# Kernel optimization log

Measured on AMD Instinct MI355X. Metric: run time of the kernel, lower is better.

## Reference

```python
import jax, jax.numpy as jnp
import numpy as np
from jax import lax


def _dense_image_warp(img, flow):
    # TFA semantics: out[b,i,j] = bilinear_sample(img[b], (i - flow[b,i,j,0], j - flow[b,i,j,1]))
    # floors clamped to [0, size-2]; alphas clamped to [0, 1].
    B, H, W, C = img.shape
    gy = jnp.arange(H, dtype=flow.dtype)[None, :, None]
    gx = jnp.arange(W, dtype=flow.dtype)[None, None, :]
    qy = gy - flow[..., 0]
    qx = gx - flow[..., 1]
    fy = jnp.clip(jnp.floor(qy), 0.0, H - 2)
    fx = jnp.clip(jnp.floor(qx), 0.0, W - 2)
    ay = jnp.clip(qy - fy, 0.0, 1.0)[..., None]
    ax = jnp.clip(qx - fx, 0.0, 1.0)[..., None]
    fy = fy.astype(jnp.int32)
    fx = fx.astype(jnp.int32)
    b = jnp.arange(B)[:, None, None]
    tl = img[b, fy, fx]
    tr = img[b, fy, fx + 1]
    bl = img[b, fy + 1, fx]
    br = img[b, fy + 1, fx + 1]
    top = tl + ax * (tr - tl)
    bot = bl + ax * (br - bl)
    return top + ay * (bot - top)


def _conv(x, w, b, act):
    y = lax.conv_general_dilated(x, w, (1, 1), 'SAME',
                                 dimension_numbers=('NHWC', 'HWIO', 'NHWC')) + b
    return jax.nn.relu(y) if act else y


def _predict(x, ws, bs):
    for i in range(4):
        x = _conv(x, ws[i], bs[i], True)
    return _conv(x, ws[4], bs[4], False)  # final 1x1 -> 2 channels, linear


def _upsample2x(x):
    B, H, W, C = x.shape
    return jax.image.resize(x, (B, 2 * H, 2 * W, C), method='bilinear')


# Conv stack dims: in=64 (concat of two 32-ch maps)
_KSHAPES = [(3, 3, 64, 32), (3, 3, 32, 64), (1, 1, 64, 64), (1, 1, 64, 16), (1, 1, 16, 2)]


def setup_inputs() -> dict:
    key = jax.random.key(0)
    ks = jax.random.split(key, 4 + 2 * len(_KSHAPES))
    B, H, W, C = 8, 256, 256, 32
    inp = {
        'input_1': jax.random.normal(ks[0], (B, H, W, C), jnp.float32),
        'input_2': jax.random.normal(ks[1], (B, H, W, C), jnp.float32),
        'flow_1_2': jax.random.normal(ks[2], (B, H, W, 2), jnp.float32) * 3.0,
        'flow_2_1': jax.random.normal(ks[3], (B, H, W, 2), jnp.float32) * 3.0,
    }
    for i, sh in enumerate(_KSHAPES):
        inp[f'w12_{i}'] = jax.random.normal(ks[4 + i], sh, jnp.float32) * 0.05
        inp[f'b12_{i}'] = jnp.zeros((sh[-1],), jnp.float32)
        inp[f'w21_{i}'] = jax.random.normal(ks[4 + len(_KSHAPES) + i], sh, jnp.float32) * 0.05
        inp[f'b21_{i}'] = jnp.zeros((sh[-1],), jnp.float32)
    return inp


def reference(input_1, input_2, flow_1_2, flow_2_1,
              w12_0, b12_0, w12_1, b12_1, w12_2, b12_2, w12_3, b12_3, w12_4, b12_4,
              w21_0, b21_0, w21_1, b21_1, w21_2, b21_2, w21_3, b21_3, w21_4, b21_4):
    ws12 = [w12_0, w12_1, w12_2, w12_3, w12_4]
    bs12 = [b12_0, b12_1, b12_2, b12_3, b12_4]
    ws21 = [w21_0, w21_1, w21_2, w21_3, w21_4]
    bs21 = [b21_0, b21_1, b21_2, b21_3, b21_4]

    # 1 -> 2 direction
    input_1_warped_1 = _dense_image_warp(input_1, flow_1_2)
    flow_change_1_2 = _predict(jnp.concatenate([input_2, input_1_warped_1], axis=3), ws12, bs12)
    flow_1_2_changed = flow_1_2 + flow_change_1_2
    input_1_warped_2 = _dense_image_warp(input_1, flow_1_2_changed)
    flow_1_2_up = _upsample2x(flow_1_2_changed)

    # 2 -> 1 direction
    input_2_warped_1 = _dense_image_warp(input_2, flow_2_1)
    flow_change_2_1 = _predict(jnp.concatenate([input_1, input_2_warped_1], axis=3), ws21, bs21)
    flow_2_1_changed = flow_2_1 + flow_change_2_1
    input_2_warped_2 = _dense_image_warp(input_2, flow_2_1_changed)
    flow_2_1_up = _upsample2x(flow_2_1_changed)

    return (input_1_warped_2, input_2_warped_2, flow_1_2_up, flow_2_1_up)
```

## Files before the change

kernel.cpp:

```cpp
#include <hip/hip_runtime.h>
#include <hip/hip_bf16.h>
#include <cstddef>

#define B_ 8
#define H_ 256
#define W_ 256

static constexpr int NPIX = B_ * H_ * W_;

typedef __attribute__((ext_vector_type(8))) short bf16x8;
typedef __attribute__((ext_vector_type(4))) float f32x4;

__device__ __forceinline__ float4 ld4(const float* p) { return *(const float4*)p; }

__device__ __forceinline__ short f2bf(float x) {
    unsigned u = __float_as_uint(x);
    unsigned r = (u + 0x7fffu + ((u >> 16) & 1u)) >> 16;
    return (short)r;
}

__global__ __launch_bounds__(256) void cvt_inputs_kernel(
    const float* __restrict__ in1, const float* __restrict__ in2,
    short* __restrict__ xb1, short* __restrict__ xb2)
{
    int t = blockIdx.x * 256 + threadIdx.x;
    const int N8 = NPIX * 32 / 8;
    const float* src = (t < N8) ? in1 : in2;
    short* dst = (t < N8) ? xb1 : xb2;
    int i = (t < N8) ? t : t - N8;
    float4 a = ld4(src + (size_t)i * 8);
    float4 b = ld4(src + (size_t)i * 8 + 4);
    bf16x8 r;
    r[0] = f2bf(a.x); r[1] = f2bf(a.y); r[2] = f2bf(a.z); r[3] = f2bf(a.w);
    r[4] = f2bf(b.x); r[5] = f2bf(b.y); r[6] = f2bf(b.z); r[7] = f2bf(b.w);
    *(bf16x8*)(dst + (size_t)i * 8) = r;
}

__global__ __launch_bounds__(256) void prep_weights_kernel(
    const float* __restrict__ w0a, const float* __restrict__ w1a,
    const float* __restrict__ w2a, const float* __restrict__ w3a,
    const float* __restrict__ w0b, const float* __restrict__ w1b,
    const float* __restrict__ w2b, const float* __restrict__ w3b,
    short* __restrict__ wt0, short* __restrict__ wt1)
{
    int t = blockIdx.x * 256 + threadIdx.x;
    if (t >= 2 * 5248) return;
    int dir = t / 5248;
    int r = t % 5248;
    const float* w0 = dir ? w0b : w0a;
    const float* w1 = dir ? w1b : w1a;
    const float* w2 = dir ? w2b : w2a;
    const float* w3 = dir ? w3b : w3a;
    short* wt = dir ? wt1 : wt0;
    bf16x8 v;
    if (r < 2304) {
        int l = r & 63, n = (r >> 6) & 1, c = (r >> 7) & 1, tp = r >> 8;
#pragma unroll
        for (int j = 0; j < 8; ++j) {
            int ci = c * 32 + 8 * (l >> 4) + j;
            int co = n * 16 + (l & 15);
            v[j] = f2bf(w0[(size_t)(tp * 64 + ci) * 32 + co]);
        }
    } else if (r < 4608) {
        int q = r - 2304;
        int l = q & 63, n = (q >> 6) & 3, tp = q >> 8;
#pragma unroll
        for (int j = 0; j < 8; ++j) {
            int ci = 8 * (l >> 4) + j;
            int co = n * 16 + (l & 15);
            v[j] = f2bf(w1[(size_t)(tp * 32 + ci) * 64 + co]);
        }
    } else if (r < 5120) {
        int q = r - 4608;
        int l = q & 63, n = (q >> 6) & 3, c = q >> 8;
#pragma unroll
        for (int j = 0; j < 8; ++j) {
            int k = 32 * c + 8 * (l >> 4) + j;
            int co = n * 16 + (l & 15);
            v[j] = f2bf(w2[(size_t)k * 64 + co]);
        }
    } else {
        int q = r - 5120;
        int l = q & 63, c = q >> 6;
#pragma unroll
        for (int j = 0; j < 8; ++j) {
            int k = 32 * c + 8 * (l >> 4) + j;
            v[j] = f2bf(w3[(size_t)k * 16 + (l & 15)]);
        }
    }
    *(bf16x8*)(wt + (size_t)r * 8) = v;
}

__global__ __launch_bounds__(256) void warp_bf16_kernel(
    const float* __restrict__ in1, const float* __restrict__ in2,
    const float* __restrict__ fl12, const float* __restrict__ fl21,
    short* __restrict__ wbf)
{
    int gid = blockIdx.x * 256 + threadIdx.x;
    int d   = (gid >= NPIX * 8);
    int g2  = gid - (d ? NPIX * 8 : 0);
    const float* img  = d ? in2 : in1;
    const float* flow = d ? fl21 : fl12;
    short* out = wbf + (size_t)d * NPIX * 32;

    int p   = g2 >> 3;
    int c4  = (g2 & 7) << 2;
    int b   = p >> 16;
    int i   = (p >> 8) & 255;
    int j   = p & 255;
    float2 f = *(const float2*)(flow + (size_t)p * 2);
    float qy = (float)i - f.x;
    float qx = (float)j - f.y;
    float fyf = fminf(fmaxf(floorf(qy), 0.0f), (float)(H_ - 2));
    float fxf = fminf(fmaxf(floorf(qx), 0.0f), (float)(W_ - 2));
    float ay = fminf(fmaxf(qy - fyf, 0.0f), 1.0f);
    float ax = fminf(fmaxf(qx - fxf, 0.0f), 1.0f);
    int fy = (int)fyf, fx = (int)fxf;
    const float* base = img + ((((size_t)b * H_ + fy) * W_ + fx) << 5) + c4;
    float4 tl = ld4(base);
    float4 tr = ld4(base + 32);
    float4 bl = ld4(base + W_ * 32);
    float4 br = ld4(base + W_ * 32 + 32);
    short4 r;
    { float t = tl.x + ax * (tr.x - tl.x); float u = bl.x + ax * (br.x - bl.x); r.x = f2bf(t + ay * (u - t)); }
    { float t = tl.y + ax * (tr.y - tl.y); float u = bl.y + ax * (br.y - bl.y); r.y = f2bf(t + ay * (u - t)); }
    { float t = tl.z + ax * (tr.z - tl.z); float u = bl.z + ax * (br.z - bl.z); r.z = f2bf(t + ay * (u - t)); }
    { float t = tl.w + ax * (tr.w - tl.w); float u = bl.w + ax * (br.w - bl.w); r.w = f2bf(t + ay * (u - t)); }
    *(short4*)(out + ((size_t)p << 5) + c4) = r;
}

__global__ __launch_bounds__(256) void warp_f32_kernel(
    const float* __restrict__ in1, const float* __restrict__ in2,
    const float* __restrict__ fcb, float* __restrict__ outf)
{
    int gid = blockIdx.x * 256 + threadIdx.x;
    int d   = (gid >= NPIX * 8);
    int g2  = gid - (d ? NPIX * 8 : 0);
    const float* img  = d ? in2 : in1;
    const float* flow = fcb + (size_t)d * NPIX * 2;
    float* out = outf + (size_t)d * NPIX * 32;

    int p   = g2 >> 3;
    int c4  = (g2 & 7) << 2;
    int b   = p >> 16;
    int i   = (p >> 8) & 255;
    int j   = p & 255;
    float2 f = *(const float2*)(flow + (size_t)p * 2);
    float qy = (float)i - f.x;
    float qx = (float)j - f.y;
    float fyf = fminf(fmaxf(floorf(qy), 0.0f), (float)(H_ - 2));
    float fxf = fminf(fmaxf(floorf(qx), 0.0f), (float)(W_ - 2));
    float ay = fminf(fmaxf(qy - fyf, 0.0f), 1.0f);
    float ax = fminf(fmaxf(qx - fxf, 0.0f), 1.0f);
    int fy = (int)fyf, fx = (int)fxf;
    const float* base = img + ((((size_t)b * H_ + fy) * W_ + fx) << 5) + c4;
    float4 tl = ld4(base);
    float4 tr = ld4(base + 32);
    float4 bl = ld4(base + W_ * 32);
    float4 br = ld4(base + W_ * 32 + 32);
    float4 r;
    { float t = tl.x + ax * (tr.x - tl.x); float u = bl.x + ax * (br.x - bl.x); r.x = t + ay * (u - t); }
    { float t = tl.y + ax * (tr.y - tl.y); float u = bl.y + ax * (br.y - bl.y); r.y = t + ay * (u - t); }
    { float t = tl.z + ax * (tr.z - tl.z); float u = bl.z + ax * (br.z - bl.z); r.z = t + ay * (u - t); }
    { float t = tl.w + ax * (tr.w - tl.w); float u = bl.w + ax * (br.w - bl.w); r.w = t + ay * (u - t); }
    *(float4*)(out + ((size_t)p << 5) + c4) = r;
}

__global__ __launch_bounds__(512) void conv0_mfma_kernel(
    const short* __restrict__ xb1, const short* __restrict__ xb2,
    const short* __restrict__ wbf,
    const short* __restrict__ wt0, const short* __restrict__ wt1,
    const float* __restrict__ b0a, const float* __restrict__ b0b,
    short* __restrict__ h0)
{
    __shared__ short swt[2304 * 8];
    int d   = blockIdx.x >> 11;
    int bid = blockIdx.x & 2047;
    const short* xoth = d ? xb1 : xb2;
    const short* xw   = wbf + (size_t)d * NPIX * 32;
    const short* wtab = d ? wt1 : wt0;
    const float* bias = d ? b0b : b0a;
    short* out = h0 + (size_t)d * NPIX * 32;

    int tid = threadIdx.x;
    for (int i = tid; i < 2304; i += 512)
        ((bf16x8*)swt)[i] = ((const bf16x8*)wtab)[i];
    __syncthreads();

    int wave = tid >> 6, lane = tid & 63;
    int l15 = lane & 15, g = lane >> 4;
    int prow = bid * 256;
    int y    = bid & 255;
    int t0   = prow + wave * 32;
    int xl0  = wave * 32 + l15;
    int xl1  = xl0 + 16;

    const short* a0p = xoth + ((size_t)(t0 + l15) << 5) + g * 8;
    const short* a1p = a0p + (16 << 5);
    const short* b0p = xw + ((size_t)(t0 + l15) << 5) + g * 8;
    const short* b1p = b0p + (16 << 5);
    const bf16x8* wfrag = (const bf16x8*)swt;

    float bv0 = bias[l15], bv1 = bias[16 + l15];
    f32x4 acc00 = {bv0, bv0, bv0, bv0};
    f32x4 acc01 = {bv1, bv1, bv1, bv1};
    f32x4 acc10 = {bv0, bv0, bv0, bv0};
    f32x4 acc11 = {bv1, bv1, bv1, bv1};
    const bf16x8 z8 = {0, 0, 0, 0, 0, 0, 0, 0};

#pragma unroll
    for (int dy = -1; dy <= 1; ++dy) {
        if ((unsigned)(y + dy) >= (unsigned)H_) continue;
#pragma unroll
        for (int dx = -1; dx <= 1; ++dx) {
            bool v0 = (unsigned)(xl0 + dx) < (unsigned)W_;
            bool v1 = (unsigned)(xl1 + dx) < (unsigned)W_;
            int off0 = (dy * W_ + (v0 ? dx : 0)) << 5;
            int off1 = (dy * W_ + (v1 ? dx : 0)) << 5;
            bf16x8 aA0 = *(const bf16x8*)(a0p + off0);
            bf16x8 aB0 = *(const bf16x8*)(b0p + off0);
            bf16x8 aA1 = *(const bf16x8*)(a1p + off1);
            bf16x8 aB1 = *(const bf16x8*)(b1p + off1);
            aA0 = v0 ? aA0 : z8;  aB0 = v0 ? aB0 : z8;
            aA1 = v1 ? aA1 : z8;  aB1 = v1 ? aB1 : z8;
            int t = (dy + 1) * 3 + (dx + 1);
            bf16x8 w0 = wfrag[(t * 4 + 0) * 64 + lane];
            bf16x8 w1 = wfrag[(t * 4 + 1) * 64 + lane];
            bf16x8 w2 = wfrag[(t * 4 + 2) * 64 + lane];
            bf16x8 w3 = wfrag[(t * 4 + 3) * 64 + lane];
            acc00 = __builtin_amdgcn_mfma_f32_16x16x32_bf16(aA0, w0, acc00, 0, 0, 0);
            acc01 = __builtin_amdgcn_mfma_f32_16x16x32_bf16(aA0, w1, acc01, 0, 0, 0);
            acc10 = __builtin_amdgcn_mfma_f32_16x16x32_bf16(aA1, w0, acc10, 0, 0, 0);
            acc11 = __builtin_amdgcn_mfma_f32_16x16x32_bf16(aA1, w1, acc11, 0, 0, 0);
            acc00 = __builtin_amdgcn_mfma_f32_16x16x32_bf16(aB0, w2, acc00, 0, 0, 0);
            acc01 = __builtin_amdgcn_mfma_f32_16x16x32_bf16(aB0, w3, acc01, 0, 0, 0);
            acc10 = __builtin_amdgcn_mfma_f32_16x16x32_bf16(aB1, w2, acc10, 0, 0, 0);
            acc11 = __builtin_amdgcn_mfma_f32_16x16x32_bf16(aB1, w3, acc11, 0, 0, 0);
        }
    }

#pragma unroll
    for (int r = 0; r < 4; ++r) {
        size_t r0 = (size_t)(t0 + g * 4 + r) << 5;
        size_t r1 = (size_t)(t0 + 16 + g * 4 + r) << 5;
        out[r0 + l15]      = f2bf(fmaxf(acc00[r], 0.f));
        out[r0 + 16 + l15] = f2bf(fmaxf(acc01[r], 0.f));
        out[r1 + l15]      = f2bf(fmaxf(acc10[r], 0.f));
        out[r1 + 16 + l15] = f2bf(fmaxf(acc11[r], 0.f));
    }
}

__global__ __launch_bounds__(512) void conv1_mfma_kernel(
    const short* __restrict__ h0,
    const short* __restrict__ wt0, const short* __restrict__ wt1,
    const float* __restrict__ b1a, const float* __restrict__ b1b,
    const float* __restrict__ b2a, const float* __restrict__ b2b,
    const float* __restrict__ b3a, const float* __restrict__ b3b,
    const float* __restrict__ w4a, const float* __restrict__ w4b,
    const float* __restrict__ b4a, const float* __restrict__ b4b,
    const float* __restrict__ fl12, const float* __restrict__ fl21,
    float* __restrict__ fcb)
{
    __shared__ short swt[2944 * 8];
    __shared__ __align__(16) short sx[8][2048];
    int d   = blockIdx.x >> 11;
    int bid = blockIdx.x & 2047;
    const short* hsrc = h0 + (size_t)d * NPIX * 32;
    const short* wtab = (d ? wt1 : wt0) + 2304 * 8;
    const float* b1 = d ? b1b : b1a;
    const float* b2 = d ? b2b : b2a;
    const float* b3 = d ? b3b : b3a;
    const float* w4 = d ? w4b : w4a;
    const float* b4 = d ? b4b : b4a;
    const float* flow = d ? fl21 : fl12;
    float* fc = fcb + (size_t)d * NPIX * 2;

    int tid = threadIdx.x;
    for (int i = tid; i < 2944; i += 512)
        ((bf16x8*)swt)[i] = ((const bf16x8*)wtab)[i];
    __syncthreads();

    int wave = tid >> 6, lane = tid & 63;
    int l15 = lane & 15, g = lane >> 4;
    int prow = bid * 256;
    int y    = bid & 255;
    int t0   = prow + wave * 32;
    int xl0  = wave * 32 + l15;
    int xl1  = xl0 + 16;

    const short* a0p = hsrc + ((size_t)(t0 + l15) << 5) + g * 8;
    const short* a1p = a0p + (16 << 5);
    const bf16x8* W1 = (const bf16x8*)swt;
    const bf16x8* W2 = (const bf16x8*)swt + 2304;
    const bf16x8* W3 = (const bf16x8*)swt + 2816;
    char* xb = (char*)&sx[wave][0];
    const bf16x8 z8 = {0, 0, 0, 0, 0, 0, 0, 0};

    f32x4 acc0[4], acc1[4];
#pragma unroll
    for (int n = 0; n < 4; ++n) {
        float b = b1[n * 16 + l15];
        acc0[n] = (f32x4){b, b, b, b};
        acc1[n] = (f32x4){b, b, b, b};
    }
#pragma unroll
    for (int dy = -1; dy <= 1; ++dy) {
        if ((unsigned)(y + dy) >= (unsigned)H_) continue;
#pragma unroll
        for (int dx = -1; dx <= 1; ++dx) {
            bool v0 = (unsigned)(xl0 + dx) < (unsigned)W_;
            bool v1 = (unsigned)(xl1 + dx) < (unsigned)W_;
            int off0 = (dy * W_ + (v0 ? dx : 0)) << 5;
            int off1 = (dy * W_ + (v1 ? dx : 0)) << 5;
            bf16x8 a0 = *(const bf16x8*)(a0p + off0);
            bf16x8 a1 = *(const bf16x8*)(a1p + off1);
            a0 = v0 ? a0 : z8;
            a1 = v1 ? a1 : z8;
            int t = (dy + 1) * 3 + (dx + 1);
#pragma unroll
            for (int n = 0; n < 4; ++n) {
                bf16x8 w = W1[(t * 4 + n) * 64 + lane];
                acc0[n] = __builtin_amdgcn_mfma_f32_16x16x32_bf16(a0, w, acc0[n], 0, 0, 0);
                acc1[n] = __builtin_amdgcn_mfma_f32_16x16x32_bf16(a1, w, acc1[n], 0, 0, 0);
            }
        }
    }
#pragma unroll
    for (int n = 0; n < 4; ++n)
#pragma unroll
        for (int r = 0; r < 4; ++r) {
            int row0 = g * 4 + r, ch = n * 16 + l15;
            int by0 = (row0 * 128 + ch * 2) ^ ((row0 & 7) << 4);
            int by1 = ((row0 + 16) * 128 + ch * 2) ^ ((row0 & 7) << 4);
            *(short*)(xb + by0) = f2bf(fmaxf(acc0[n][r], 0.f));
            *(short*)(xb + by1) = f2bf(fmaxf(acc1[n][r], 0.f));
        }

#pragma unroll
    for (int n = 0; n < 4; ++n) {
        float b = b2[n * 16 + l15];
        acc0[n] = (f32x4){b, b, b, b};
        acc1[n] = (f32x4){b, b, b, b};
    }
#pragma unroll
    for (int c = 0; c < 2; ++c) {
        int by0 = (l15 * 128 + (32 * c + 8 * g) * 2) ^ ((l15 & 7) << 4);
        int by1 = ((l15 + 16) * 128 + (32 * c + 8 * g) * 2) ^ ((l15 & 7) << 4);
        bf16x8 a0 = *(const bf16x8*)(xb + by0);
        bf16x8 a1 = *(const bf16x8*)(xb + by1);
#pragma unroll
        for (int n = 0; n < 4; ++n) {
            bf16x8 w = W2[(c * 4 + n) * 64 + lane];
            acc0[n] = __builtin_amdgcn_mfma_f32_16x16x32_bf16(a0, w, acc0[n], 0, 0, 0);
            acc1[n] = __builtin_amdgcn_mfma_f32_16x16x32_bf16(a1, w, acc1[n], 0, 0, 0);
        }
    }
#pragma unroll
    for (int n = 0; n < 4; ++n)
#pragma unroll
        for (int r = 0; r < 4; ++r) {
            int row0 = g * 4 + r, ch = n * 16 + l15;
            int by0 = (row0 * 128 + ch * 2) ^ ((row0 & 7) << 4);
            int by1 = ((row0 + 16) * 128 + ch * 2) ^ ((row0 & 7) << 4);
            *(short*)(xb + by0) = f2bf(fmaxf(acc0[n][r], 0.f));
            *(short*)(xb + by1) = f2bf(fmaxf(acc1[n][r], 0.f));
        }

    float b3v = b3[l15];
    f32x4 acc3a = {b3v, b3v, b3v, b3v};
    f32x4 acc3b = {b3v, b3v, b3v, b3v};
#pragma unroll
    for (int c = 0; c < 2; ++c) {
        int by0 = (l15 * 128 + (32 * c + 8 * g) * 2) ^ ((l15 & 7) << 4);
        int by1 = ((l15 + 16) * 128 + (32 * c + 8 * g) * 2) ^ ((l15 & 7) << 4);
        bf16x8 a0 = *(const bf16x8*)(xb + by0);
        bf16x8 a1 = *(const bf16x8*)(xb + by1);
        bf16x8 w = W3[c * 64 + lane];
        acc3a = __builtin_amdgcn_mfma_f32_16x16x32_bf16(a0, w, acc3a, 0, 0, 0);
        acc3b = __builtin_amdgcn_mfma_f32_16x16x32_bf16(a1, w, acc3b, 0, 0, 0);
    }

    float w40 = w4[l15 * 2 + 0], w41 = w4[l15 * 2 + 1];
    float bb0 = b4[0], bb1 = b4[1];
#pragma unroll
    for (int tt = 0; tt < 2; ++tt) {
        f32x4 a3 = tt ? acc3b : acc3a;
#pragma unroll
        for (int r = 0; r < 4; ++r) {
            float v = fmaxf(a3[r], 0.f);
            float s0 = v * w40, s1 = v * w41;
#pragma unroll
            for (int m = 1; m < 16; m <<= 1) {
                s0 += __shfl_xor(s0, m);
                s1 += __shfl_xor(s1, m);
            }
            if (l15 == 0) {
                int pr = t0 + tt * 16 + g * 4 + r;
                float2 fl = *(const float2*)(flow + (size_t)pr * 2);
                float2 o; o.x = fl.x + bb0 + s0; o.y = fl.y + bb1 + s1;
                *(float2*)(fc + (size_t)pr * 2) = o;
            }
        }
    }
}

__global__ __launch_bounds__(256) void upsample_kernel(
    const float* __restrict__ fcb, float* __restrict__ outup)
{
    int gid = blockIdx.x * 256 + threadIdx.x;
    const int NUP = B_ * 512 * 512;
    int d  = (gid >= NUP);
    int g2 = gid - (d ? NUP : 0);
    const float* fc = fcb + (size_t)d * NPIX * 2;
    float* out = outup + (size_t)d * NUP * 2;

    int b  = g2 >> 18;
    int oy = (g2 >> 9) & 511;
    int ox = g2 & 511;
    float iy = 0.5f * (float)oy - 0.25f;
    float ix = 0.5f * (float)ox - 0.25f;
    float y0f = floorf(iy), x0f = floorf(ix);
    float wy = iy - y0f, wx = ix - x0f;
    int y0 = min(max((int)y0f, 0), H_ - 1);
    int y1 = min(max((int)y0f + 1, 0), H_ - 1);
    int x0 = min(max((int)x0f, 0), W_ - 1);
    int x1 = min(max((int)x0f + 1, 0), W_ - 1);
    float2 v00 = *(const float2*)(fc + (((size_t)b * H_ + y0) * W_ + x0) * 2);
    float2 v01 = *(const float2*)(fc + (((size_t)b * H_ + y0) * W_ + x1) * 2);
    float2 v10 = *(const float2*)(fc + (((size_t)b * H_ + y1) * W_ + x0) * 2);
    float2 v11 = *(const float2*)(fc + (((size_t)b * H_ + y1) * W_ + x1) * 2);
    float2 r;
    { float t = v00.x + wx * (v01.x - v00.x); float u = v10.x + wx * (v11.x - v10.x); r.x = t + wy * (u - t); }
    { float t = v00.y + wx * (v01.y - v00.y); float u = v10.y + wx * (v11.y - v10.y); r.y = t + wy * (u - t); }
    *(float2*)(out + (size_t)g2 * 2) = r;
}

extern "C" void kernel_launch(void* const* d_in, const int* in_sizes, int n_in,
                              void* d_out, int out_size, void* d_ws, size_t ws_size,
                              hipStream_t stream)
{
    (void)in_sizes; (void)n_in; (void)out_size; (void)ws_size;
    const float* input1 = (const float*)d_in[0];
    const float* input2 = (const float*)d_in[1];
    const float* fl12 = (const float*)d_in[2];
    const float* fl21 = (const float*)d_in[3];
    char* wsb = (char*)d_ws;
    short* xb1  = (short*)(wsb);
    short* xb2  = (short*)(wsb + 33554432);
    short* wbf  = (short*)(wsb + 67108864);
    short* h0   = (short*)(wsb + 134217728);
    float* fcb  = (float*)(wsb + 201326592);
    short* wt0  = (short*)(wsb + 209715200);
    short* wt1  = (short*)(wsb + 209715200 + 5248 * 16);
    float* outf = (float*)d_out;
    float* outup = outf + (size_t)2 * NPIX * 32;

    cvt_inputs_kernel<<<NPIX * 64 / 8 / 256, 256, 0, stream>>>(input1, input2, xb1, xb2);
    prep_weights_kernel<<<(2 * 5248 + 255) / 256, 256, 0, stream>>>(
        (const float*)d_in[4],  (const float*)d_in[8],  (const float*)d_in[12], (const float*)d_in[16],
        (const float*)d_in[6],  (const float*)d_in[10], (const float*)d_in[14], (const float*)d_in[18],
        wt0, wt1);
    warp_bf16_kernel<<<2 * NPIX * 8 / 256, 256, 0, stream>>>(input1, input2, fl12, fl21, wbf);
    conv0_mfma_kernel<<<2 * NPIX / 256, 512, 0, stream>>>(
        xb1, xb2, wbf, wt0, wt1,
        (const float*)d_in[5], (const float*)d_in[7], h0);
    conv1_mfma_kernel<<<2 * NPIX / 256, 512, 0, stream>>>(
        h0, wt0, wt1,
        (const float*)d_in[9],  (const float*)d_in[11],
        (const float*)d_in[13], (const float*)d_in[15],
        (const float*)d_in[17], (const float*)d_in[19],
        (const float*)d_in[20], (const float*)d_in[22],
        (const float*)d_in[21], (const float*)d_in[23],
        fl12, fl21, fcb);
    warp_f32_kernel<<<2 * NPIX * 8 / 256, 256, 0, stream>>>(input1, input2, fcb, outf);
    upsample_kernel<<<2 * B_ * 512 * 512 / 256, 256, 0, stream>>>(fcb, outup);
}
```

Measured before the change: 593.2 us.

## Merge pre/post elementwise kernels into single launches and swizzle conv blocks across XCDs

Combines the input conversion, weight prep and first warp into one pre_kernel, and the final warp and upsample into one post_kernel. Each block picks its role from its block index. This cuts launches from seven to four and lets independent memory-bound work share the GPU, removing tail gaps between kernels. It also remaps conv block indices so consecutive rows land on the same XCD, which is meant to improve L2 reuse of neighbouring rows; the fused kernels may lose some per-kernel tuning.

Result: faster. 581.1 us (-2.0%).

```diff
diff --git a/kernel.cpp b/kernel.cpp
--- a/kernel.cpp
+++ b/kernel.cpp
@@ -19,84 +19,11 @@
     return (short)r;
 }
 
-__global__ __launch_bounds__(256) void cvt_inputs_kernel(
-    const float* __restrict__ in1, const float* __restrict__ in2,
-    short* __restrict__ xb1, short* __restrict__ xb2)
-{
-    int t = blockIdx.x * 256 + threadIdx.x;
-    const int N8 = NPIX * 32 / 8;
-    const float* src = (t < N8) ? in1 : in2;
-    short* dst = (t < N8) ? xb1 : xb2;
-    int i = (t < N8) ? t : t - N8;
-    float4 a = ld4(src + (size_t)i * 8);
-    float4 b = ld4(src + (size_t)i * 8 + 4);
-    bf16x8 r;
-    r[0] = f2bf(a.x); r[1] = f2bf(a.y); r[2] = f2bf(a.z); r[3] = f2bf(a.w);
-    r[4] = f2bf(b.x); r[5] = f2bf(b.y); r[6] = f2bf(b.z); r[7] = f2bf(b.w);
-    *(bf16x8*)(dst + (size_t)i * 8) = r;
-}
-
-__global__ __launch_bounds__(256) void prep_weights_kernel(
-    const float* __restrict__ w0a, const float* __restrict__ w1a,
-    const float* __restrict__ w2a, const float* __restrict__ w3a,
-    const float* __restrict__ w0b, const float* __restrict__ w1b,
-    const float* __restrict__ w2b, const float* __restrict__ w3b,
-    short* __restrict__ wt0, short* __restrict__ wt1)
-{
-    int t = blockIdx.x * 256 + threadIdx.x;
-    if (t >= 2 * 5248) return;
-    int dir = t / 5248;
-    int r = t % 5248;
-    const float* w0 = dir ? w0b : w0a;
-    const float* w1 = dir ? w1b : w1a;
-    const float* w2 = dir ? w2b : w2a;
-    const float* w3 = dir ? w3b : w3a;
-    short* wt = dir ? wt1 : wt0;
-    bf16x8 v;
-    if (r < 2304) {
-        int l = r & 63, n = (r >> 6) & 1, c = (r >> 7) & 1, tp = r >> 8;
-#pragma unroll
-        for (int j = 0; j < 8; ++j) {
-            int ci = c * 32 + 8 * (l >> 4) + j;
-            int co = n * 16 + (l & 15);
-            v[j] = f2bf(w0[(size_t)(tp * 64 + ci) * 32 + co]);
-        }
-    } else if (r < 4608) {
-        int q = r - 2304;
-        int l = q & 63, n = (q >> 6) & 3, tp = q >> 8;
-#pragma unroll
-        for (int j = 0; j < 8; ++j) {
-            int ci = 8 * (l >> 4) + j;
-            int co = n * 16 + (l & 15);
-            v[j] = f2bf(w1[(size_t)(tp * 32 + ci) * 64 + co]);
-        }
-    } else if (r < 5120) {
-        int q = r - 4608;
-        int l = q & 63, n = (q >> 6) & 3, c = q >> 8;
-#pragma unroll
-        for (int j = 0; j < 8; ++j) {
-            int k = 32 * c + 8 * (l >> 4) + j;
-            int co = n * 16 + (l & 15);
-            v[j] = f2bf(w2[(size_t)k * 64 + co]);
-        }
-    } else {
-        int q = r - 5120;
-        int l = q & 63, c = q >> 6;
-#pragma unroll
-        for (int j = 0; j < 8; ++j) {
-            int k = 32 * c + 8 * (l >> 4) + j;
-            v[j] = f2bf(w3[(size_t)k * 16 + (l & 15)]);
-        }
-    }
-    *(bf16x8*)(wt + (size_t)r * 8) = v;
-}
-
-__global__ __launch_bounds__(256) void warp_bf16_kernel(
-    const float* __restrict__ in1, const float* __restrict__ in2,
+__device__ __forceinline__ void warp_bf16_body(
+    int gid, const float* __restrict__ in1, const float* __restrict__ in2,
     const float* __restrict__ fl12, const float* __restrict__ fl21,
     short* __restrict__ wbf)
 {
-    int gid = blockIdx.x * 256 + threadIdx.x;
     int d   = (gid >= NPIX * 8);
     int g2  = gid - (d ? NPIX * 8 : 0);
     const float* img  = d ? in2 : in1;
@@ -129,11 +56,348 @@
     *(short4*)(out + ((size_t)p << 5) + c4) = r;
 }
 
-__global__ __launch_bounds__(256) void warp_f32_kernel(
+__device__ __forceinline__ void cvt_body(
+    int t, const float* __restrict__ in1, const float* __restrict__ in2,
+    short* __restrict__ xb1, short* __restrict__ xb2)
+{
+    const int N8 = NPIX * 32 / 8;
+    const float* src = (t < N8) ? in1 : in2;
+    short* dst = (t < N8) ? xb1 : xb2;
+    int i = (t < N8) ? t : t - N8;
+    float4 a = ld4(src + (size_t)i * 8);
+    float4 b = ld4(src + (size_t)i * 8 + 4);
+    bf16x8 r;
+    r[0] = f2bf(a.x); r[1] = f2bf(a.y); r[2] = f2bf(a.z); r[3] = f2bf(a.w);
+    r[4] = f2bf(b.x); r[5] = f2bf(b.y); r[6] = f2bf(b.z); r[7] = f2bf(b.w);
+    *(bf16x8*)(dst + (size_t)i * 8) = r;
+}
+
+__device__ __forceinline__ void prep_body(
+    int t,
+    const float* __restrict__ w0a, const float* __restrict__ w1a,
+    const float* __restrict__ w2a, const float* __restrict__ w3a,
+    const float* __restrict__ w0b, const float* __restrict__ w1b,
+    const float* __restrict__ w2b, const float* __restrict__ w3b,
+    short* __restrict__ wt0, short* __restrict__ wt1)
+{
+    if (t >= 2 * 5248) return;
+    int dir = t / 5248;
+    int r = t % 5248;
+    const float* w0 = dir ? w0b : w0a;
+    const float* w1 = dir ? w1b : w1a;
+    const float* w2 = dir ? w2b : w2a;
+    const float* w3 = dir ? w3b : w3a;
+    short* wt = dir ? wt1 : wt0;
+    bf16x8 v;
+    if (r < 2304) {
+        int l = r & 63, n = (r >> 6) & 1, c = (r >> 7) & 1, tp = r >> 8;
+#pragma unroll
+        for (int j = 0; j < 8; ++j) {
+            int ci = c * 32 + 8 * (l >> 4) + j;
+            int co = n * 16 + (l & 15);
+            v[j] = f2bf(w0[(size_t)(tp * 64 + ci) * 32 + co]);
+        }
+    } else if (r < 4608) {
+        int q = r - 2304;
+        int l = q & 63, n = (q >> 6) & 3, tp = q >> 8;
+#pragma unroll
+        for (int j = 0; j < 8; ++j) {
+            int ci = 8 * (l >> 4) + j;
+            int co = n * 16 + (l & 15);
+            v[j] = f2bf(w1[(size_t)(tp * 32 + ci) * 64 + co]);
+        }
+    } else if (r < 5120) {
+        int q = r - 4608;
+        int l = q & 63, n = (q >> 6) & 3, c = q >> 8;
+#pragma unroll
+        for (int j = 0; j < 8; ++j) {
+            int k = 32 * c + 8 * (l >> 4) + j;
+            int co = n * 16 + (l & 15);
+            v[j] = f2bf(w2[(size_t)k * 64 + co]);
+        }
+    } else {
+        int q = r - 5120;
+        int l = q & 63, c = q >> 6;
+#pragma unroll
+        for (int j = 0; j < 8; ++j) {
+            int k = 32 * c + 8 * (l >> 4) + j;
+            v[j] = f2bf(w3[(size_t)k * 16 + (l & 15)]);
+        }
+    }
+    *(bf16x8*)(wt + (size_t)r * 8) = v;
+}
+
+__global__ __launch_bounds__(256) void pre_kernel(
     const float* __restrict__ in1, const float* __restrict__ in2,
+    const float* __restrict__ fl12, const float* __restrict__ fl21,
+    short* __restrict__ xb1, short* __restrict__ xb2, short* __restrict__ wbf,
+    const float* __restrict__ w0a, const float* __restrict__ w1a,
+    const float* __restrict__ w2a, const float* __restrict__ w3a,
+    const float* __restrict__ w0b, const float* __restrict__ w1b,
+    const float* __restrict__ w2b, const float* __restrict__ w3b,
+    short* __restrict__ wt0, short* __restrict__ wt1)
+{
+    const int NW = 2 * NPIX * 8 / 256;
+    const int NC = NPIX * 64 / 8 / 256;
+    int blk = blockIdx.x;
+    if (blk < NW) {
+        warp_bf16_body(blk * 256 + threadIdx.x, in1, in2, fl12, fl21, wbf);
+    } else if (blk < NW + NC) {
+        cvt_body((blk - NW) * 256 + threadIdx.x, in1, in2, xb1, xb2);
+    } else {
+        prep_body((blk - NW - NC) * 256 + threadIdx.x,
+                  w0a, w1a, w2a, w3a, w0b, w1b, w2b, w3b, wt0, wt1);
+    }
+}
+
+__device__ __forceinline__ int xcd_swz(int orig) {
+    return (orig & 7) * 512 + (orig >> 3);
+}
+
+__global__ __launch_bounds__(512) void conv0_mfma_kernel(
+    const short* __restrict__ xb1, const short* __restrict__ xb2,
+    const short* __restrict__ wbf,
+    const short* __restrict__ wt0, const short* __restrict__ wt1,
+    const float* __restrict__ b0a, const float* __restrict__ b0b,
+    short* __restrict__ h0)
+{
+    __shared__ short swt[2304 * 8];
+    int wg  = xcd_swz(blockIdx.x);
+    int d   = wg >> 11;
+    int bid = wg & 2047;
+    const short* xoth = d ? xb1 : xb2;
+    const short* xw   = wbf + (size_t)d * NPIX * 32;
+    const short* wtab = d ? wt1 : wt0;
+    const float* bias = d ? b0b : b0a;
+    short* out = h0 + (size_t)d * NPIX * 32;
+
+    int tid = threadIdx.x;
+    for (int i = tid; i < 2304; i += 512)
+        ((bf16x8*)swt)[i] = ((const bf16x8*)wtab)[i];
+    __syncthreads();
+
+    int wave = tid >> 6, lane = tid & 63;
+    int l15 = lane & 15, g = lane >> 4;
+    int prow = bid * 256;
+    int y    = bid & 255;
+    int t0   = prow + wave * 32;
+    int xl0  = wave * 32 + l15;
+    int xl1  = xl0 + 16;
+
+    const short* a0p = xoth + ((size_t)(t0 + l15) << 5) + g * 8;
+    const short* a1p = a0p + (16 << 5);
+    const short* b0p = xw + ((size_t)(t0 + l15) << 5) + g * 8;
+    const short* b1p = b0p + (16 << 5);
+    const bf16x8* wfrag = (const bf16x8*)swt;
+
+    float bv0 = bias[l15], bv1 = bias[16 + l15];
+    f32x4 acc00 = {bv0, bv0, bv0, bv0};
+    f32x4 acc01 = {bv1, bv1, bv1, bv1};
+    f32x4 acc10 = {bv0, bv0, bv0, bv0};
+    f32x4 acc11 = {bv1, bv1, bv1, bv1};
+    const bf16x8 z8 = {0, 0, 0, 0, 0, 0, 0, 0};
+
+#pragma unroll
+    for (int dy = -1; dy <= 1; ++dy) {
+        if ((unsigned)(y + dy) >= (unsigned)H_) continue;
+#pragma unroll
+        for (int dx = -1; dx <= 1; ++dx) {
+            bool v0 = (unsigned)(xl0 + dx) < (unsigned)W_;
+            bool v1 = (unsigned)(xl1 + dx) < (unsigned)W_;
+            int off0 = (dy * W_ + (v0 ? dx : 0)) << 5;
+            int off1 = (dy * W_ + (v1 ? dx : 0)) << 5;
+            bf16x8 aA0 = *(const bf16x8*)(a0p + off0);
+            bf16x8 aB0 = *(const bf16x8*)(b0p + off0);
+            bf16x8 aA1 = *(const bf16x8*)(a1p + off1);
+            bf16x8 aB1 = *(const bf16x8*)(b1p + off1);
+            aA0 = v0 ? aA0 : z8;  aB0 = v0 ? aB0 : z8;
+            aA1 = v1 ? aA1 : z8;  aB1 = v1 ? aB1 : z8;
+            int t = (dy + 1) * 3 + (dx + 1);
+            bf16x8 w0 = wfrag[(t * 4 + 0) * 64 + lane];
+            bf16x8 w1 = wfrag[(t * 4 + 1) * 64 + lane];
+            bf16x8 w2 = wfrag[(t * 4 + 2) * 64 + lane];
+            bf16x8 w3 = wfrag[(t * 4 + 3) * 64 + lane];
+            acc00 = __builtin_amdgcn_mfma_f32_16x16x32_bf16(aA0, w0, acc00, 0, 0, 0);
+            acc01 = __builtin_amdgcn_mfma_f32_16x16x32_bf16(aA0, w1, acc01, 0, 0, 0);
+            acc10 = __builtin_amdgcn_mfma_f32_16x16x32_bf16(aA1, w0, acc10, 0, 0, 0);
+            acc11 = __builtin_amdgcn_mfma_f32_16x16x32_bf16(aA1, w1, acc11, 0, 0, 0);
+            acc00 = __builtin_amdgcn_mfma_f32_16x16x32_bf16(aB0, w2, acc00, 0, 0, 0);
+            acc01 = __builtin_amdgcn_mfma_f32_16x16x32_bf16(aB0, w3, acc01, 0, 0, 0);
+            acc10 = __builtin_amdgcn_mfma_f32_16x16x32_bf16(aB1, w2, acc10, 0, 0, 0);
+            acc11 = __builtin_amdgcn_mfma_f32_16x16x32_bf16(aB1, w3, acc11, 0, 0, 0);
+        }
+    }
+
+#pragma unroll
+    for (int r = 0; r < 4; ++r) {
+        size_t r0 = (size_t)(t0 + g * 4 + r) << 5;
+        size_t r1 = (size_t)(t0 + 16 + g * 4 + r) << 5;
+        out[r0 + l15]      = f2bf(fmaxf(acc00[r], 0.f));
+        out[r0 + 16 + l15] = f2bf(fmaxf(acc01[r], 0.f));
+        out[r1 + l15]      = f2bf(fmaxf(acc10[r], 0.f));
+        out[r1 + 16 + l15] = f2bf(fmaxf(acc11[r], 0.f));
+    }
+}
+
+__global__ __launch_bounds__(512) void conv1_mfma_kernel(
+    const short* __restrict__ h0,
+    const short* __restrict__ wt0, const short* __restrict__ wt1,
+    const float* __restrict__ b1a, const float* __restrict__ b1b,
+    const float* __restrict__ b2a, const float* __restrict__ b2b,
+    const float* __restrict__ b3a, const float* __restrict__ b3b,
+    const float* __restrict__ w4a, const float* __restrict__ w4b,
+    const float* __restrict__ b4a, const float* __restrict__ b4b,
+    const float* __restrict__ fl12, const float* __restrict__ fl21,
+    float* __restrict__ fcb)
+{
+    __shared__ short swt[2944 * 8];
+    __shared__ __align__(16) short sx[8][2048];
+    int wg  = xcd_swz(blockIdx.x);
+    int d   = wg >> 11;
+    int bid = wg & 2047;
+    const short* hsrc = h0 + (size_t)d * NPIX * 32;
+    const short* wtab = (d ? wt1 : wt0) + 2304 * 8;
+    const float* b1 = d ? b1b : b1a;
+    const float* b2 = d ? b2b : b2a;
+    const float* b3 = d ? b3b : b3a;
+    const float* w4 = d ? w4b : w4a;
+    const float* b4 = d ? b4b : b4a;
+    const float* flow = d ? fl21 : fl12;
+    float* fc = fcb + (size_t)d * NPIX * 2;
+
+    int tid = threadIdx.x;
+    for (int i = tid; i < 2944; i += 512)
+        ((bf16x8*)swt)[i] = ((const bf16x8*)wtab)[i];
+    __syncthreads();
+
+    int wave = tid >> 6, lane = tid & 63;
+    int l15 = lane & 15, g = lane >> 4;
+    int prow = bid * 256;
+    int y    = bid & 255;
+    int t0   = prow + wave * 32;
+    int xl0  = wave * 32 + l15;
+    int xl1  = xl0 + 16;
+
+    const short* a0p = hsrc + ((size_t)(t0 + l15) << 5) + g * 8;
+    const short* a1p = a0p + (16 << 5);
+    const bf16x8* W1 = (const bf16x8*)swt;
+    const bf16x8* W2 = (const bf16x8*)swt + 2304;
+    const bf16x8* W3 = (const bf16x8*)swt + 2816;
+    char* xb = (char*)&sx[wave][0];
+    const bf16x8 z8 = {0, 0, 0, 0, 0, 0, 0, 0};
+
+    f32x4 acc0[4], acc1[4];
+#pragma unroll
+    for (int n = 0; n < 4; ++n) {
+        float b = b1[n * 16 + l15];
+        acc0[n] = (f32x4){b, b, b, b};
+        acc1[n] = (f32x4){b, b, b, b};
+    }
+#pragma unroll
+    for (int dy = -1; dy <= 1; ++dy) {
+        if ((unsigned)(y + dy) >= (unsigned)H_) continue;
+#pragma unroll
+        for (int dx = -1; dx <= 1; ++dx) {
+            bool v0 = (unsigned)(xl0 + dx) < (unsigned)W_;
+            bool v1 = (unsigned)(xl1 + dx) < (unsigned)W_;
+            int off0 = (dy * W_ + (v0 ? dx : 0)) << 5;
+            int off1 = (dy * W_ + (v1 ? dx : 0)) << 5;
+            bf16x8 a0 = *(const bf16x8*)(a0p + off0);
+            bf16x8 a1 = *(const bf16x8*)(a1p + off1);
+            a0 = v0 ? a0 : z8;
+            a1 = v1 ? a1 : z8;
+            int t = (dy + 1) * 3 + (dx + 1);
+#pragma unroll
+            for (int n = 0; n < 4; ++n) {
+                bf16x8 w = W1[(t * 4 + n) * 64 + lane];
+                acc0[n] = __builtin_amdgcn_mfma_f32_16x16x32_bf16(a0, w, acc0[n], 0, 0, 0);
+                acc1[n] = __builtin_amdgcn_mfma_f32_16x16x32_bf16(a1, w, acc1[n], 0, 0, 0);
+            }
+        }
+    }
+#pragma unroll
+    for (int n = 0; n < 4; ++n)
+#pragma unroll
+        for (int r = 0; r < 4; ++r) {
+            int row0 = g * 4 + r, ch = n * 16 + l15;
+            int by0 = (row0 * 128 + ch * 2) ^ ((row0 & 7) << 4);
+            int by1 = ((row0 + 16) * 128 + ch * 2) ^ ((row0 & 7) << 4);
+            *(short*)(xb + by0) = f2bf(fmaxf(acc0[n][r], 0.f));
+            *(short*)(xb + by1) = f2bf(fmaxf(acc1[n][r], 0.f));
+        }
+
+#pragma unroll
+    for (int n = 0; n < 4; ++n) {
+        float b = b2[n * 16 + l15];
+        acc0[n] = (f32x4){b, b, b, b};
+        acc1[n] = (f32x4){b, b, b, b};
+    }
+#pragma unroll
+    for (int c = 0; c < 2; ++c) {
+        int by0 = (l15 * 128 + (32 * c + 8 * g) * 2) ^ ((l15 & 7) << 4);
+        int by1 = ((l15 + 16) * 128 + (32 * c + 8 * g) * 2) ^ ((l15 & 7) << 4);
+        bf16x8 a0 = *(const bf16x8*)(xb + by0);
+        bf16x8 a1 = *(const bf16x8*)(xb + by1);
+#pragma unroll
+        for (int n = 0; n < 4; ++n) {
+            bf16x8 w = W2[(c * 4 + n) * 64 + lane];
+            acc0[n] = __builtin_amdgcn_mfma_f32_16x16x32_bf16(a0, w, acc0[n], 0, 0, 0);
+            acc1[n] = __builtin_amdgcn_mfma_f32_16x16x32_bf16(a1, w, acc1[n], 0, 0, 0);
+        }
+    }
+#pragma unroll
+    for (int n = 0; n < 4; ++n)
+#pragma unroll
+        for (int r = 0; r < 4; ++r) {
+            int row0 = g * 4 + r, ch = n * 16 + l15;
+            int by0 = (row0 * 128 + ch * 2) ^ ((row0 & 7) << 4);
+            int by1 = ((row0 + 16) * 128 + ch * 2) ^ ((row0 & 7) << 4);
+            *(short*)(xb + by0) = f2bf(fmaxf(acc0[n][r], 0.f));
+            *(short*)(xb + by1) = f2bf(fmaxf(acc1[n][r], 0.f));
+        }
+
+    float b3v = b3[l15];
+    f32x4 acc3a = {b3v, b3v, b3v, b3v};
+    f32x4 acc3b = {b3v, b3v, b3v, b3v};
+#pragma unroll
+    for (int c = 0; c < 2; ++c) {
+        int by0 = (l15 * 128 + (32 * c + 8 * g) * 2) ^ ((l15 & 7) << 4);
+        int by1 = ((l15 + 16) * 128 + (32 * c + 8 * g) * 2) ^ ((l15 & 7) << 4);
+        bf16x8 a0 = *(const bf16x8*)(xb + by0);
+        bf16x8 a1 = *(const bf16x8*)(xb + by1);
+        bf16x8 w = W3[c * 64 + lane];
+        acc3a = __builtin_amdgcn_mfma_f32_16x16x32_bf16(a0, w, acc3a, 0, 0, 0);
+        acc3b = __builtin_amdgcn_mfma_f32_16x16x32_bf16(a1, w, acc3b, 0, 0, 0);
+    }
+
+    float w40 = w4[l15 * 2 + 0], w41 = w4[l15 * 2 + 1];
+    float bb0 = b4[0], bb1 = b4[1];
+#pragma unroll
+    for (int tt = 0; tt < 2; ++tt) {
+        f32x4 a3 = tt ? acc3b : acc3a;
+#pragma unroll
+        for (int r = 0; r < 4; ++r) {
+            float v = fmaxf(a3[r], 0.f);
+            float s0 = v * w40, s1 = v * w41;
+#pragma unroll
+            for (int m = 1; m < 16; m <<= 1) {
+                s0 += __shfl_xor(s0, m);
+                s1 += __shfl_xor(s1, m);
+            }
+            if (l15 == 0) {
+                int pr = t0 + tt * 16 + g * 4 + r;
+                float2 fl = *(const float2*)(flow + (size_t)pr * 2);
+                float2 o; o.x = fl.x + bb0 + s0; o.y = fl.y + bb1 + s1;
+                *(float2*)(fc + (size_t)pr * 2) = o;
+            }
+        }
+    }
+}
+
+__device__ __forceinline__ void warp_f32_body(
+    int gid, const float* __restrict__ in1, const float* __restrict__ in2,
     const float* __restrict__ fcb, float* __restrict__ outf)
 {
-    int gid = blockIdx.x * 256 + threadIdx.x;
     int d   = (gid >= NPIX * 8);
     int g2  = gid - (d ? NPIX * 8 : 0);
     const float* img  = d ? in2 : in1;
@@ -166,248 +430,9 @@
     *(float4*)(out + ((size_t)p << 5) + c4) = r;
 }
 
-__global__ __launch_bounds__(512) void conv0_mfma_kernel(
-    const short* __restrict__ xb1, const short* __restrict__ xb2,
-    const short* __restrict__ wbf,
-    const short* __restrict__ wt0, const short* __restrict__ wt1,
-    const float* __restrict__ b0a, const float* __restrict__ b0b,
-    short* __restrict__ h0)
-{
-    __shared__ short swt[2304 * 8];
-    int d   = blockIdx.x >> 11;
-    int bid = blockIdx.x & 2047;
-    const short* xoth = d ? xb1 : xb2;
-    const short* xw   = wbf + (size_t)d * NPIX * 32;
-    const short* wtab = d ? wt1 : wt0;
-    const float* bias = d ? b0b : b0a;
-    short* out = h0 + (size_t)d * NPIX * 32;
-
-    int tid = threadIdx.x;
-    for (int i = tid; i < 2304; i += 512)
-        ((bf16x8*)swt)[i] = ((const bf16x8*)wtab)[i];
-    __syncthreads();
-
-    int wave = tid >> 6, lane = tid & 63;
-    int l15 = lane & 15, g = lane >> 4;
-    int prow = bid * 256;
-    int y    = bid & 255;
-    int t0   = prow + wave * 32;
-    int xl0  = wave * 32 + l15;
-    int xl1  = xl0 + 16;
-
-    const short* a0p = xoth + ((size_t)(t0 + l15) << 5) + g * 8;
-    const short* a1p = a0p + (16 << 5);
-    const short* b0p = xw + ((size_t)(t0 + l15) << 5) + g * 8;
-    const short* b1p = b0p + (16 << 5);
-    const bf16x8* wfrag = (const bf16x8*)swt;
-
-    float bv0 = bias[l15], bv1 = bias[16 + l15];
-    f32x4 acc00 = {bv0, bv0, bv0, bv0};
-    f32x4 acc01 = {bv1, bv1, bv1, bv1};
-    f32x4 acc10 = {bv0, bv0, bv0, bv0};
-    f32x4 acc11 = {bv1, bv1, bv1, bv1};
-    const bf16x8 z8 = {0, 0, 0, 0, 0, 0, 0, 0};
-
-#pragma unroll
-    for (int dy = -1; dy <= 1; ++dy) {
-        if ((unsigned)(y + dy) >= (unsigned)H_) continue;
-#pragma unroll
-        for (int dx = -1; dx <= 1; ++dx) {
-            bool v0 = (unsigned)(xl0 + dx) < (unsigned)W_;
-            bool v1 = (unsigned)(xl1 + dx) < (unsigned)W_;
-            int off0 = (dy * W_ + (v0 ? dx : 0)) << 5;
-            int off1 = (dy * W_ + (v1 ? dx : 0)) << 5;
-            bf16x8 aA0 = *(const bf16x8*)(a0p + off0);
-            bf16x8 aB0 = *(const bf16x8*)(b0p + off0);
-            bf16x8 aA1 = *(const bf16x8*)(a1p + off1);
-            bf16x8 aB1 = *(const bf16x8*)(b1p + off1);
-            aA0 = v0 ? aA0 : z8;  aB0 = v0 ? aB0 : z8;
-            aA1 = v1 ? aA1 : z8;  aB1 = v1 ? aB1 : z8;
-            int t = (dy + 1) * 3 + (dx + 1);
-            bf16x8 w0 = wfrag[(t * 4 + 0) * 64 + lane];
-            bf16x8 w1 = wfrag[(t * 4 + 1) * 64 + lane];
-            bf16x8 w2 = wfrag[(t * 4 + 2) * 64 + lane];
-            bf16x8 w3 = wfrag[(t * 4 + 3) * 64 + lane];
-            acc00 = __builtin_amdgcn_mfma_f32_16x16x32_bf16(aA0, w0, acc00, 0, 0, 0);
-            acc01 = __builtin_amdgcn_mfma_f32_16x16x32_bf16(aA0, w1, acc01, 0, 0, 0);
-            acc10 = __builtin_amdgcn_mfma_f32_16x16x32_bf16(aA1, w0, acc10, 0, 0, 0);
-            acc11 = __builtin_amdgcn_mfma_f32_16x16x32_bf16(aA1, w1, acc11, 0, 0, 0);
-            acc00 = __builtin_amdgcn_mfma_f32_16x16x32_bf16(aB0, w2, acc00, 0, 0, 0);
-            acc01 = __builtin_amdgcn_mfma_f32_16x16x32_bf16(aB0, w3, acc01, 0, 0, 0);
-            acc10 = __builtin_amdgcn_mfma_f32_16x16x32_bf16(aB1, w2, acc10, 0, 0, 0);
-            acc11 = __builtin_amdgcn_mfma_f32_16x16x32_bf16(aB1, w3, acc11, 0, 0, 0);
-        }
-    }
-
-#pragma unroll
-    for (int r = 0; r < 4; ++r) {
-        size_t r0 = (size_t)(t0 + g * 4 + r) << 5;
-        size_t r1 = (size_t)(t0 + 16 + g * 4 + r) << 5;
-        out[r0 + l15]      = f2bf(fmaxf(acc00[r], 0.f));
-        out[r0 + 16 + l15] = f2bf(fmaxf(acc01[r], 0.f));
-        out[r1 + l15]      = f2bf(fmaxf(acc10[r], 0.f));
-        out[r1 + 16 + l15] = f2bf(fmaxf(acc11[r], 0.f));
-    }
-}
-
-__global__ __launch_bounds__(512) void conv1_mfma_kernel(
-    const short* __restrict__ h0,
-    const short* __restrict__ wt0, const short* __restrict__ wt1,
-    const float* __restrict__ b1a, const float* __restrict__ b1b,
-    const float* __restrict__ b2a, const float* __restrict__ b2b,
-    const float* __restrict__ b3a, const float* __restrict__ b3b,
-    const float* __restrict__ w4a, const float* __restrict__ w4b,
-    const float* __restrict__ b4a, const float* __restrict__ b4b,
-    const float* __restrict__ fl12, const float* __restrict__ fl21,
-    float* __restrict__ fcb)
-{
-    __shared__ short swt[2944 * 8];
-    __shared__ __align__(16) short sx[8][2048];
-    int d   = blockIdx.x >> 11;
-    int bid = blockIdx.x & 2047;
-    const short* hsrc = h0 + (size_t)d * NPIX * 32;
-    const short* wtab = (d ? wt1 : wt0) + 2304 * 8;
-    const float* b1 = d ? b1b : b1a;
-    const float* b2 = d ? b2b : b2a;
-    const float* b3 = d ? b3b : b3a;
-    const float* w4 = d ? w4b : w4a;
-    const float* b4 = d ? b4b : b4a;
-    const float* flow = d ? fl21 : fl12;
-    float* fc = fcb + (size_t)d * NPIX * 2;
-
-    int tid = threadIdx.x;
-    for (int i = tid; i < 2944; i += 512)
-        ((bf16x8*)swt)[i] = ((const bf16x8*)wtab)[i];
-    __syncthreads();
-
-    int wave = tid >> 6, lane = tid & 63;
-    int l15 = lane & 15, g = lane >> 4;
-    int prow = bid * 256;
-    int y    = bid & 255;
-    int t0   = prow + wave * 32;
-    int xl0  = wave * 32 + l15;
-    int xl1  = xl0 + 16;
-
-    const short* a0p = hsrc + ((size_t)(t0 + l15) << 5) + g * 8;
-    const short* a1p = a0p + (16 << 5);
-    const bf16x8* W1 = (const bf16x8*)swt;
-    const bf16x8* W2 = (const bf16x8*)swt + 2304;
-    const bf16x8* W3 = (const bf16x8*)swt + 2816;
-    char* xb = (char*)&sx[wave][0];
-    const bf16x8 z8 = {0, 0, 0, 0, 0, 0, 0, 0};
-
-    f32x4 acc0[4], acc1[4];
-#pragma unroll
-    for (int n = 0; n < 4; ++n) {
-        float b = b1[n * 16 + l15];
-        acc0[n] = (f32x4){b, b, b, b};
-        acc1[n] = (f32x4){b, b, b, b};
-    }
-#pragma unroll
-    for (int dy = -1; dy <= 1; ++dy) {
-        if ((unsigned)(y + dy) >= (unsigned)H_) continue;
-#pragma unroll
-        for (int dx = -1; dx <= 1; ++dx) {
-            bool v0 = (unsigned)(xl0 + dx) < (unsigned)W_;
-            bool v1 = (unsigned)(xl1 + dx) < (unsigned)W_;
-            int off0 = (dy * W_ + (v0 ? dx : 0)) << 5;
-            int off1 = (dy * W_ + (v1 ? dx : 0)) << 5;
-            bf16x8 a0 = *(const bf16x8*)(a0p + off0);
-            bf16x8 a1 = *(const bf16x8*)(a1p + off1);
-            a0 = v0 ? a0 : z8;
-            a1 = v1 ? a1 : z8;
-            int t = (dy + 1) * 3 + (dx + 1);
-#pragma unroll
-            for (int n = 0; n < 4; ++n) {
-                bf16x8 w = W1[(t * 4 + n) * 64 + lane];
-                acc0[n] = __builtin_amdgcn_mfma_f32_16x16x32_bf16(a0, w, acc0[n], 0, 0, 0);
-                acc1[n] = __builtin_amdgcn_mfma_f32_16x16x32_bf16(a1, w, acc1[n], 0, 0, 0);
-            }
-        }
-    }
-#pragma unroll
-    for (int n = 0; n < 4; ++n)
-#pragma unroll
-        for (int r = 0; r < 4; ++r) {
-            int row0 = g * 4 + r, ch = n * 16 + l15;
-            int by0 = (row0 * 128 + ch * 2) ^ ((row0 & 7) << 4);
-            int by1 = ((row0 + 16) * 128 + ch * 2) ^ ((row0 & 7) << 4);
-            *(short*)(xb + by0) = f2bf(fmaxf(acc0[n][r], 0.f));
-            *(short*)(xb + by1) = f2bf(fmaxf(acc1[n][r], 0.f));
-        }
-
-#pragma unroll
-    for (int n = 0; n < 4; ++n) {
-        float b = b2[n * 16 + l15];
-        acc0[n] = (f32x4){b, b, b, b};
-        acc1[n] = (f32x4){b, b, b, b};
-    }
-#pragma unroll
-    for (int c = 0; c < 2; ++c) {
-        int by0 = (l15 * 128 + (32 * c + 8 * g) * 2) ^ ((l15 & 7) << 4);
-        int by1 = ((l15 + 16) * 128 + (32 * c + 8 * g) * 2) ^ ((l15 & 7) << 4);
-        bf16x8 a0 = *(const bf16x8*)(xb + by0);
-        bf16x8 a1 = *(const bf16x8*)(xb + by1);
-#pragma unroll
-        for (int n = 0; n < 4; ++n) {
-            bf16x8 w = W2[(c * 4 + n) * 64 + lane];
-            acc0[n] = __builtin_amdgcn_mfma_f32_16x16x32_bf16(a0, w, acc0[n], 0, 0, 0);
-            acc1[n] = __builtin_amdgcn_mfma_f32_16x16x32_bf16(a1, w, acc1[n], 0, 0, 0);
-        }
-    }
-#pragma unroll
-    for (int n = 0; n < 4; ++n)
-#pragma unroll
-        for (int r = 0; r < 4; ++r) {
-            int row0 = g * 4 + r, ch = n * 16 + l15;
-            int by0 = (row0 * 128 + ch * 2) ^ ((row0 & 7) << 4);
-            int by1 = ((row0 + 16) * 128 + ch * 2) ^ ((row0 & 7) << 4);
-            *(short*)(xb + by0) = f2bf(fmaxf(acc0[n][r], 0.f));
-            *(short*)(xb + by1) = f2bf(fmaxf(acc1[n][r], 0.f));
-        }
-
-    float b3v = b3[l15];
-    f32x4 acc3a = {b3v, b3v, b3v, b3v};
-    f32x4 acc3b = {b3v, b3v, b3v, b3v};
-#pragma unroll
-    for (int c = 0; c < 2; ++c) {
-        int by0 = (l15 * 128 + (32 * c + 8 * g) * 2) ^ ((l15 & 7) << 4);
-        int by1 = ((l15 + 16) * 128 + (32 * c + 8 * g) * 2) ^ ((l15 & 7) << 4);
-        bf16x8 a0 = *(const bf16x8*)(xb + by0);
-        bf16x8 a1 = *(const bf16x8*)(xb + by1);
-        bf16x8 w = W3[c * 64 + lane];
-        acc3a = __builtin_amdgcn_mfma_f32_16x16x32_bf16(a0, w, acc3a, 0, 0, 0);
-        acc3b = __builtin_amdgcn_mfma_f32_16x16x32_bf16(a1, w, acc3b, 0, 0, 0);
-    }
-
-    float w40 = w4[l15 * 2 + 0], w41 = w4[l15 * 2 + 1];
-    float bb0 = b4[0], bb1 = b4[1];
-#pragma unroll
-    for (int tt = 0; tt < 2; ++tt) {
-        f32x4 a3 = tt ? acc3b : acc3a;
-#pragma unroll
-        for (int r = 0; r < 4; ++r) {
-            float v = fmaxf(a3[r], 0.f);
-            float s0 = v * w40, s1 = v * w41;
-#pragma unroll
-            for (int m = 1; m < 16; m <<= 1) {
-                s0 += __shfl_xor(s0, m);
-                s1 += __shfl_xor(s1, m);
-            }
-            if (l15 == 0) {
-                int pr = t0 + tt * 16 + g * 4 + r;
-                float2 fl = *(const float2*)(flow + (size_t)pr * 2);
-                float2 o; o.x = fl.x + bb0 + s0; o.y = fl.y + bb1 + s1;
-                *(float2*)(fc + (size_t)pr * 2) = o;
-            }
-        }
-    }
-}
-
-__global__ __launch_bounds__(256) void upsample_kernel(
-    const float* __restrict__ fcb, float* __restrict__ outup)
-{
-    int gid = blockIdx.x * 256 + threadIdx.x;
+__device__ __forceinline__ void upsample_body(
+    int gid, const float* __restrict__ fcb, float* __restrict__ outup)
+{
     const int NUP = B_ * 512 * 512;
     int d  = (gid >= NUP);
     int g2 = gid - (d ? NUP : 0);
@@ -435,6 +460,20 @@
     *(float2*)(out + (size_t)g2 * 2) = r;
 }
 
+__global__ __launch_bounds__(256) void post_kernel(
+    const float* __restrict__ in1, const float* __restrict__ in2,
+    const float* __restrict__ fcb, float* __restrict__ outf,
+    float* __restrict__ outup)
+{
+    const int NWF = 2 * NPIX * 8 / 256;
+    int blk = blockIdx.x;
+    if (blk < NWF) {
+        warp_f32_body(blk * 256 + threadIdx.x, in1, in2, fcb, outf);
+    } else {
+        upsample_body((blk - NWF) * 256 + threadIdx.x, fcb, outup);
+    }
+}
+
 extern "C" void kernel_launch(void* const* d_in, const int* in_sizes, int n_in,
                               void* d_out, int out_size, void* d_ws, size_t ws_size,
                               hipStream_t stream)
@@ -455,12 +494,12 @@
     float* outf = (float*)d_out;
     float* outup = outf + (size_t)2 * NPIX * 32;
 
-    cvt_inputs_kernel<<<NPIX * 64 / 8 / 256, 256, 0, stream>>>(input1, input2, xb1, xb2);
-    prep_weights_kernel<<<(2 * 5248 + 255) / 256, 256, 0, stream>>>(
+    const int NPRE = 2 * NPIX * 8 / 256 + NPIX * 64 / 8 / 256 + (2 * 5248 + 255) / 256;
+    pre_kernel<<<NPRE, 256, 0, stream>>>(
+        input1, input2, fl12, fl21, xb1, xb2, wbf,
         (const float*)d_in[4],  (const float*)d_in[8],  (const float*)d_in[12], (const float*)d_in[16],
         (const float*)d_in[6],  (const float*)d_in[10], (const float*)d_in[14], (const float*)d_in[18],
         wt0, wt1);
-    warp_bf16_kernel<<<2 * NPIX * 8 / 256, 256, 0, stream>>>(input1, input2, fl12, fl21, wbf);
     conv0_mfma_kernel<<<2 * NPIX / 256, 512, 0, stream>>>(
         xb1, xb2, wbf, wt0, wt1,
         (const float*)d_in[5], (const float*)d_in[7], h0);
@@ -472,6 +511,6 @@
         (const float*)d_in[20], (const float*)d_in[22],
         (const float*)d_in[21], (const float*)d_in[23],
         fl12, fl21, fcb);
-    warp_f32_kernel<<<2 * NPIX * 8 / 256, 256, 0, stream>>>(input1, input2, fcb, outf);
-    upsample_kernel<<<2 * B_ * 512 * 512 / 256, 256, 0, stream>>>(fcb, outup);
-}
+    const int NPOST = 2 * NPIX * 8 / 256 + 2 * B_ * 512 * 512 / 256;
+    post_kernel<<<NPOST, 256, 0, stream>>>(input1, input2, fcb, outf, outup);
+}
```
